# Kernel optimization log

Measured on AMD Instinct MI355X. Metric: run time of the kernel, lower is better.

## Reference

```python
import math
import jax, jax.numpy as jnp
import numpy as np

N = 50000
C = 128      # in_channels == out_channels
H = 8        # nhead
D = C // H   # head_dim = 16
E = 800000


def _layernorm(x, g, b, eps=1e-5):
    mu = jnp.mean(x, axis=-1, keepdims=True)
    var = jnp.var(x, axis=-1, keepdims=True)
    return (x - mu) * jax.lax.rsqrt(var + eps) * g + b


def setup_inputs() -> dict:
    key = jax.random.key(0)
    ks = jax.random.split(key, 12)
    s = 1.0 / math.sqrt(C)          # ~xavier scale
    s4 = 1.0 / math.sqrt(4 * C)
    return {
        "x": jax.random.normal(ks[0], (N, C), dtype=jnp.float32),
        "edge_index": jax.random.randint(ks[1], (2, E), 0, N, dtype=jnp.int64),
        "Wq": jax.random.normal(ks[2], (C, C), dtype=jnp.float32) * s,
        "Wk": jax.random.normal(ks[3], (C, C), dtype=jnp.float32) * s,
        "Wv": jax.random.normal(ks[4], (C, C), dtype=jnp.float32) * s,
        "Wo": jax.random.normal(ks[5], (C, C), dtype=jnp.float32) * s,
        "bo": jnp.zeros((C,), dtype=jnp.float32),
        "Wf1": jax.random.normal(ks[6], (C, 4 * C), dtype=jnp.float32) * s,
        "bf1": jnp.zeros((4 * C,), dtype=jnp.float32),
        "Wf2": jax.random.normal(ks[7], (4 * C, C), dtype=jnp.float32) * s4,
        "bf2": jnp.zeros((C,), dtype=jnp.float32),
        "g1": jnp.ones((C,), dtype=jnp.float32),
        "b1": jnp.zeros((C,), dtype=jnp.float32),
        "g2": jnp.ones((C,), dtype=jnp.float32),
        "b2": jnp.zeros((C,), dtype=jnp.float32),
    }


def reference(x, edge_index, Wq, Wk, Wv, Wo, bo, Wf1, bf1, Wf2, bf2, g1, b1, g2, b2):
    n = x.shape[0]
    loops = jnp.arange(n, dtype=edge_index.dtype)
    row = jnp.concatenate([edge_index[0], loops])  # source nodes
    col = jnp.concatenate([edge_index[1], loops])  # destination nodes

    q = (x @ Wq).reshape(n, H, D)
    k = (x @ Wk).reshape(n, H, D)
    v = (x @ Wv).reshape(n, H, D)

    # edge-level attention scores [E+N, H]
    scores = jnp.einsum('ehd,ehd->eh', q[row], k[col]) / math.sqrt(D)
    smax = jax.ops.segment_max(scores, col, num_segments=n)  # every node has a self-loop
    exp = jnp.exp(scores - smax[col])
    ssum = jax.ops.segment_sum(exp, col, num_segments=n)
    alpha = exp / (ssum[col] + 1e-8)

    out = jax.ops.segment_sum(v[row] * alpha[..., None], col, num_segments=n)
    attn = out.reshape(n, C) @ Wo + bo

    residual = x  # input_proj is Identity (in_channels == out_channels)
    x1 = _layernorm(residual + attn, g1, b1)
    ffn = jax.nn.gelu(x1 @ Wf1 + bf1, approximate=False) @ Wf2 + bf2
    return _layernorm(x1 + ffn, g2, b2)
```

## Files before the change

kernel.cpp:

```cpp
#include <hip/hip_runtime.h>
#include <cmath>


typedef short bf16x8 __attribute__((ext_vector_type(8)));
typedef float f32x4 __attribute__((ext_vector_type(4)));
typedef unsigned int uint_as1 __attribute__((address_space(1)));
typedef unsigned int uint_as3 __attribute__((address_space(3)));

__device__ inline unsigned short f2bf(float f) {
    unsigned int u = __float_as_uint(f);
    u += 0x7fffu + ((u >> 16) & 1u);
    return (unsigned short)(u >> 16);
}
__device__ inline float bflo(unsigned int w) { return __uint_as_float(w << 16); }
__device__ inline float bfhi(unsigned int w) { return __uint_as_float(w & 0xffff0000u); }

__device__ inline void gload16(const unsigned short* g, unsigned short* l) {
    __builtin_amdgcn_global_load_lds((const uint_as1*)g, (uint_as3*)l, 16, 0, 0);
}


__global__ void k_zero(int* __restrict__ p, int n) {
    int i = blockIdx.x * 256 + threadIdx.x;
    if (i < n) p[i] = 0;
}

__global__ void k_count(const int* __restrict__ ei, int* __restrict__ counts,
                        int E, int N) {
    int e = blockIdx.x * 256 + threadIdx.x;
    if (e >= E + N) return;
    int col = (e < E) ? ei[E + e] : (e - E);
    atomicAdd(&counts[col], 1);
}

__global__ void k_scan1(const int* __restrict__ counts, int* __restrict__ incl,
                        int* __restrict__ bsums, int N) {
    __shared__ int s[256];
    int t = threadIdx.x, i = blockIdx.x * 256 + t;
    int v = (i < N) ? counts[i] : 0;
    s[t] = v; __syncthreads();
    for (int off = 1; off < 256; off <<= 1) {
        int add = (t >= off) ? s[t - off] : 0;
        __syncthreads();
        s[t] += add;
        __syncthreads();
    }
    if (i < N) incl[i] = s[t];
    if (t == 255) bsums[blockIdx.x] = s[255];
}

__global__ void k_scan2(const int* __restrict__ bsums, int* __restrict__ boffs, int NB) {
    __shared__ int s[256];
    int t = threadIdx.x;
    int v = (t < NB) ? bsums[t] : 0;
    s[t] = v; __syncthreads();
    for (int off = 1; off < 256; off <<= 1) {
        int add = (t >= off) ? s[t - off] : 0;
        __syncthreads();
        s[t] += add;
        __syncthreads();
    }
    if (t < NB) boffs[t] = s[t] - v;
}

__global__ void k_scan3(const int* __restrict__ incl, const int* __restrict__ counts,
                        const int* __restrict__ boffs, int* __restrict__ nstart,
                        int* __restrict__ cursor, int N) {
    int i = blockIdx.x * 256 + threadIdx.x;
    if (i >= N) return;
    int st = incl[i] - counts[i] + boffs[blockIdx.x];
    nstart[i] = st;
    cursor[i] = st;
}

__global__ void k_fill(const int* __restrict__ ei, int* __restrict__ cursor,
                       int* __restrict__ csr, int E, int N) {
    int e = blockIdx.x * 256 + threadIdx.x;
    if (e >= E + N) return;
    int row, col;
    if (e < E) { row = ei[e]; col = ei[E + e]; }
    else       { row = col = e - E; }
    int pos = atomicAdd(&cursor[col], 1);
    csr[pos] = row;
}


__global__ void k_cast(const float* __restrict__ x, unsigned short* __restrict__ xb,
                       int total4) {
    int i = blockIdx.x * 256 + threadIdx.x;
    if (i >= total4) return;
    float4 v = ((const float4*)x)[i];
    ushort4 o;
    o.x = f2bf(v.x); o.y = f2bf(v.y); o.z = f2bf(v.z); o.w = f2bf(v.w);
    ((ushort4*)xb)[i] = o;
}

__global__ void k_prep(const float* Wq, const float* Wk, const float* Wv, const float* Wo,
                       const float* Wf1, const float* Wf2,
                       unsigned short* Wqkvt, unsigned short* Wot,
                       unsigned short* Wf1t, unsigned short* Wf2t) {
    int z = blockIdx.y;
    const float* in; unsigned short* out; int K, Co;
    switch (z) {
        case 0: in = Wq;  out = Wqkvt;          K = 128; Co = 128; break;
        case 1: in = Wk;  out = Wqkvt + 16384;  K = 128; Co = 128; break;
        case 2: in = Wv;  out = Wqkvt + 32768;  K = 128; Co = 128; break;
        case 3: in = Wo;  out = Wot;            K = 128; Co = 128; break;
        case 4: in = Wf1; out = Wf1t;           K = 128; Co = 512; break;
        default: in = Wf2; out = Wf2t;          K = 512; Co = 128; break;
    }
    int idx = blockIdx.x * 256 + threadIdx.x;
    if (idx >= K * Co) return;
    int k = idx / Co, c = idx % Co;
    out[c * K + k] = f2bf(in[idx]);
}


template <int EPI>
__global__ __launch_bounds__(256) void k_gemm_big(
    const unsigned short* __restrict__ A, const unsigned short* __restrict__ Bt,
    const float* __restrict__ bias, const float* __restrict__ resid,
    const float* __restrict__ g, const float* __restrict__ b,
    float* __restrict__ outf, unsigned short* __restrict__ outb,
    int M, int K, int Cout) {
    __shared__ unsigned short As[128 * 64];
    __shared__ unsigned short Bs[128 * 64];
    __shared__ float pSum[2][128];
    __shared__ float pSq[2][128];

    int tid = threadIdx.x;
    int wid = tid >> 6, lane = tid & 63;
    int quad = lane >> 4, l16 = lane & 15;
    int wr = wid >> 1, wc = wid & 1;
    int m0 = blockIdx.x * 128;
    int n0 = blockIdx.y * 128;

    int srow = tid >> 3;
    int gch = (tid & 7) ^ (srow & 7);
    const unsigned short* gA[4];
    const unsigned short* gB[4];
#pragma unroll
    for (int j = 0; j < 4; ++j) {
        int ra = m0 + j * 32 + srow; if (ra > M - 1) ra = M - 1;
        gA[j] = A + (size_t)ra * K + gch * 8;
        gB[j] = Bt + (size_t)(n0 + j * 32 + srow) * K + gch * 8;
    }

    f32x4 acc[4][4];
#pragma unroll
    for (int i = 0; i < 4; ++i)
#pragma unroll
        for (int j = 0; j < 4; ++j) acc[i][j] = {0.f, 0.f, 0.f, 0.f};

    int KT = K >> 6;
    for (int kt = 0; kt < KT; ++kt) {
        int ko = kt * 64;
#pragma unroll
        for (int j = 0; j < 4; ++j) {
            gload16(gA[j] + ko, As + j * 2048 + tid * 8);
            gload16(gB[j] + ko, Bs + j * 2048 + tid * 8);
        }
        __syncthreads();
#pragma unroll
        for (int s = 0; s < 2; ++s) {
            int swz = ((s * 4 + quad) ^ (l16 & 7)) * 8;
            bf16x8 af[4], bfr[4];
#pragma unroll
            for (int t4 = 0; t4 < 4; ++t4) {
                af[t4]  = *(const bf16x8*)&As[(wr * 64 + t4 * 16 + l16) * 64 + swz];
                bfr[t4] = *(const bf16x8*)&Bs[(wc * 64 + t4 * 16 + l16) * 64 + swz];
            }
#pragma unroll
            for (int ti = 0; ti < 4; ++ti)
#pragma unroll
                for (int tj = 0; tj < 4; ++tj)
                    acc[ti][tj] = __builtin_amdgcn_mfma_f32_16x16x32_bf16(
                        af[ti], bfr[tj], acc[ti][tj], 0, 0, 0);
        }
        __syncthreads();
    }

    if constexpr (EPI != 2) {
#pragma unroll
        for (int ti = 0; ti < 4; ++ti)
#pragma unroll
            for (int tj = 0; tj < 4; ++tj) {
                int col = n0 + wc * 64 + tj * 16 + l16;
#pragma unroll
                for (int r = 0; r < 4; ++r) {
                    int row = m0 + wr * 64 + ti * 16 + quad * 4 + r;
                    if (row >= M) continue;
                    float v = acc[ti][tj][r];
                    if constexpr (EPI == 1) {
                        float gg = v + bias[col];
                        v = 0.5f * gg * (1.f + erff(gg * 0.70710678118f));
                    }
                    outb[(size_t)row * Cout + col] = f2bf(v);
                }
            }
    } else {
        float bi[4], gv[4], bv[4];
#pragma unroll
        for (int tj = 0; tj < 4; ++tj) {
            int col = wc * 64 + tj * 16 + l16;
            bi[tj] = bias[col]; gv[tj] = g[col]; bv[tj] = b[col];
        }
#pragma unroll
        for (int ti = 0; ti < 4; ++ti)
#pragma unroll
            for (int tj = 0; tj < 4; ++tj) {
                int col = wc * 64 + tj * 16 + l16;
#pragma unroll
                for (int r = 0; r < 4; ++r) {
                    int row = m0 + wr * 64 + ti * 16 + quad * 4 + r;
                    float rv = (row < M) ? resid[(size_t)row * 128 + col] : 0.f;
                    acc[ti][tj][r] += bi[tj] + rv;
                }
            }
#pragma unroll
        for (int ti = 0; ti < 4; ++ti)
#pragma unroll
            for (int r = 0; r < 4; ++r) {
                float s = acc[ti][0][r] + acc[ti][1][r] + acc[ti][2][r] + acc[ti][3][r];
                float q = acc[ti][0][r] * acc[ti][0][r] + acc[ti][1][r] * acc[ti][1][r]
                        + acc[ti][2][r] * acc[ti][2][r] + acc[ti][3][r] * acc[ti][3][r];
                s += __shfl_xor(s, 1); q += __shfl_xor(q, 1);
                s += __shfl_xor(s, 2); q += __shfl_xor(q, 2);
                s += __shfl_xor(s, 4); q += __shfl_xor(q, 4);
                s += __shfl_xor(s, 8); q += __shfl_xor(q, 8);
                if (l16 == 0) {
                    int lr = wr * 64 + ti * 16 + quad * 4 + r;
                    pSum[wc][lr] = s; pSq[wc][lr] = q;
                }
            }
        __syncthreads();
        if (tid < 128) {
            float s = pSum[0][tid] + pSum[1][tid];
            float q = pSq[0][tid] + pSq[1][tid];
            float mean = s * 0.0078125f;
            float var = q * 0.0078125f - mean * mean;
            pSum[0][tid] = mean;
            pSq[0][tid] = rsqrtf(var + 1e-5f);
        }
        __syncthreads();
#pragma unroll
        for (int ti = 0; ti < 4; ++ti)
#pragma unroll
            for (int r = 0; r < 4; ++r) {
                int lr = wr * 64 + ti * 16 + quad * 4 + r;
                int row = m0 + lr;
                if (row >= M) continue;
                float mean = pSum[0][lr], rs = pSq[0][lr];
#pragma unroll
                for (int tj = 0; tj < 4; ++tj) {
                    int col = wc * 64 + tj * 16 + l16;
                    float y = (acc[ti][tj][r] - mean) * rs * gv[tj] + bv[tj];
                    if (outf) outf[(size_t)row * 128 + col] = y;
                    if (outb) outb[(size_t)row * 128 + col] = f2bf(y);
                }
            }
    }
}


__global__ __launch_bounds__(256) void k_attn(
    const unsigned int* __restrict__ qkv, const int* __restrict__ nstart,
    const int* __restrict__ counts, const int* __restrict__ csr,
    unsigned int* __restrict__ ob, int N) {
    int j = blockIdx.x * 4 + (threadIdx.x >> 6);
    if (j >= N) return;
    int l = threadIdx.x & 63;

    unsigned int kw = qkv[(size_t)j * 192 + 64 + l];
    float kx = bflo(kw), ky = bfhi(kw);

    int start = nstart[j], cnt = counts[j];
    float m = -3.0e38f, lsum = 0.f, a0 = 0.f, a1 = 0.f;
    int i = 0;
    for (; i + 4 <= cnt; i += 4) {
        int r0 = csr[start + i + 0], r1 = csr[start + i + 1];
        int r2 = csr[start + i + 2], r3 = csr[start + i + 3];
        unsigned int qw0 = qkv[(size_t)r0 * 192 + l];
        unsigned int qw1 = qkv[(size_t)r1 * 192 + l];
        unsigned int qw2 = qkv[(size_t)r2 * 192 + l];
        unsigned int qw3 = qkv[(size_t)r3 * 192 + l];
        unsigned int vw0 = qkv[(size_t)r0 * 192 + 128 + l];
        unsigned int vw1 = qkv[(size_t)r1 * 192 + 128 + l];
        unsigned int vw2 = qkv[(size_t)r2 * 192 + 128 + l];
        unsigned int vw3 = qkv[(size_t)r3 * 192 + 128 + l];

        float p0 = fmaf(bflo(qw0), kx, bfhi(qw0) * ky);
        float p1 = fmaf(bflo(qw1), kx, bfhi(qw1) * ky);
        float p2 = fmaf(bflo(qw2), kx, bfhi(qw2) * ky);
        float p3 = fmaf(bflo(qw3), kx, bfhi(qw3) * ky);
        p0 += __shfl_xor(p0, 1); p1 += __shfl_xor(p1, 1);
        p2 += __shfl_xor(p2, 1); p3 += __shfl_xor(p3, 1);
        p0 += __shfl_xor(p0, 2); p1 += __shfl_xor(p1, 2);
        p2 += __shfl_xor(p2, 2); p3 += __shfl_xor(p3, 2);
        p0 += __shfl_xor(p0, 4); p1 += __shfl_xor(p1, 4);
        p2 += __shfl_xor(p2, 4); p3 += __shfl_xor(p3, 4);
        float s0 = p0 * 0.25f, s1 = p1 * 0.25f, s2 = p2 * 0.25f, s3 = p3 * 0.25f;

        float mn = fmaxf(fmaxf(fmaxf(s0, s1), fmaxf(s2, s3)), m);
        float scale = __expf(m - mn);
        float e0 = __expf(s0 - mn), e1 = __expf(s1 - mn);
        float e2 = __expf(s2 - mn), e3 = __expf(s3 - mn);
        lsum = lsum * scale + ((e0 + e1) + (e2 + e3));
        a0 = a0 * scale + e0 * bflo(vw0) + e1 * bflo(vw1) + e2 * bflo(vw2) + e3 * bflo(vw3);
        a1 = a1 * scale + e0 * bfhi(vw0) + e1 * bfhi(vw1) + e2 * bfhi(vw2) + e3 * bfhi(vw3);
        m = mn;
    }
    for (; i < cnt; ++i) {
        int r = csr[start + i];
        unsigned int qw = qkv[(size_t)r * 192 + l];
        unsigned int vw = qkv[(size_t)r * 192 + 128 + l];
        float p = fmaf(bflo(qw), kx, bfhi(qw) * ky);
        p += __shfl_xor(p, 1);
        p += __shfl_xor(p, 2);
        p += __shfl_xor(p, 4);
        float sc = p * 0.25f;
        float mn = fmaxf(m, sc);
        float scale = __expf(m - mn);
        float e = __expf(sc - mn);
        lsum = lsum * scale + e;
        a0 = a0 * scale + e * bflo(vw);
        a1 = a1 * scale + e * bfhi(vw);
        m = mn;
    }
    float inv = 1.f / (lsum + 1e-8f);
    unsigned int w = ((unsigned int)f2bf(a1 * inv) << 16) | (unsigned int)f2bf(a0 * inv);
    ob[(size_t)j * 64 + l] = w;
}


extern "C" void kernel_launch(void* const* d_in, const int* in_sizes, int n_in,
                              void* d_out, int out_size, void* d_ws, size_t ws_size,
                              hipStream_t stream) {
    const float* x   = (const float*)d_in[0];
    const int* ei    = (const int*)d_in[1];
    const float* Wq  = (const float*)d_in[2];
    const float* Wk  = (const float*)d_in[3];
    const float* Wv  = (const float*)d_in[4];
    const float* Wo  = (const float*)d_in[5];
    const float* bo  = (const float*)d_in[6];
    const float* Wf1 = (const float*)d_in[7];
    const float* bf1 = (const float*)d_in[8];
    const float* Wf2 = (const float*)d_in[9];
    const float* bf2 = (const float*)d_in[10];
    const float* g1  = (const float*)d_in[11];
    const float* b1  = (const float*)d_in[12];
    const float* g2  = (const float*)d_in[13];
    const float* b2  = (const float*)d_in[14];

    int N = in_sizes[0] / 128;
    int E = in_sizes[1] / 2;
    int N2 = ((N + 127) / 128) * 128;
    int NE = E + N;

    char* p = (char*)d_ws;
    auto alloc = [&](size_t bytes) -> char* {
        char* r = p;
        p += (bytes + 255) & ~(size_t)255;
        return r;
    };
    unsigned short* qkv = (unsigned short*)alloc((size_t)N2 * 512 * 2);
    unsigned short* ob  = qkv + (size_t)N2 * 384;
    unsigned short* hb  = qkv;
    unsigned short* x1b = (unsigned short*)alloc((size_t)N2 * 128 * 2);
    unsigned short* xb  = x1b;
    float* x1f          = (float*)alloc((size_t)N2 * 128 * 4);
    unsigned short* Wqkvt = (unsigned short*)alloc(3 * 128 * 128 * 2);
    unsigned short* Wot   = (unsigned short*)alloc(128 * 128 * 2);
    unsigned short* Wf1t  = (unsigned short*)alloc(512 * 128 * 2);
    unsigned short* Wf2t  = (unsigned short*)alloc(128 * 512 * 2);
    int* counts = (int*)alloc((size_t)N * 4);
    int* incl   = (int*)alloc((size_t)N * 4);
    int* nstart = (int*)alloc((size_t)N * 4);
    int* cursor = (int*)alloc((size_t)N * 4);
    int* bsums  = (int*)alloc(1024 * 4);
    int* boffs  = (int*)alloc(1024 * 4);
    int* csr    = (int*)alloc((size_t)NE * 4);

    int NB = (N + 255) / 256;
    int M128 = (N + 127) / 128;

    k_zero<<<NB, 256, 0, stream>>>(counts, N);
    k_count<<<(NE + 255) / 256, 256, 0, stream>>>(ei, counts, E, N);
    k_scan1<<<NB, 256, 0, stream>>>(counts, incl, bsums, N);
    k_scan2<<<1, 256, 0, stream>>>(bsums, boffs, NB);
    k_scan3<<<NB, 256, 0, stream>>>(incl, counts, boffs, nstart, cursor, N);
    k_fill<<<(NE + 255) / 256, 256, 0, stream>>>(ei, cursor, csr, E, N);

    k_cast<<<((N * 128 / 4) + 255) / 256, 256, 0, stream>>>(x, xb, N * 128 / 4);
    k_prep<<<dim3(256, 6), 256, 0, stream>>>(Wq, Wk, Wv, Wo, Wf1, Wf2,
                                             Wqkvt, Wot, Wf1t, Wf2t);

    k_gemm_big<0><<<dim3(M128, 3), 256, 0, stream>>>(
        xb, Wqkvt, nullptr, nullptr, nullptr, nullptr, nullptr, qkv, N, 128, 384);

    k_attn<<<(N + 3) / 4, 256, 0, stream>>>((const unsigned int*)qkv, nstart,
                                            counts, csr, (unsigned int*)ob, N);

    k_gemm_big<2><<<dim3(M128, 1), 256, 0, stream>>>(
        ob, Wot, bo, x, g1, b1, x1f, x1b, N, 128, 128);

    k_gemm_big<1><<<dim3(M128, 4), 256, 0, stream>>>(
        x1b, Wf1t, bf1, nullptr, nullptr, nullptr, nullptr, hb, N, 128, 512);

    k_gemm_big<2><<<dim3(M128, 1), 256, 0, stream>>>(
        hb, Wf2t, bf2, x1f, g2, b2, (float*)d_out, nullptr, N, 512, 128);
}
```

Measured before the change: 387.0 us.

## Fuse FFN up/down GEMMs into one kernel keeping hidden activations in LDS

```diff
diff --git a/kernel.cpp b/kernel.cpp
--- a/kernel.cpp
+++ b/kernel.cpp
@@ -17,6 +17,12 @@
 
 __device__ inline void gload16(const unsigned short* g, unsigned short* l) {
     __builtin_amdgcn_global_load_lds((const uint_as1*)g, (uint_as3*)l, 16, 0, 0);
+}
+
+__device__ inline bf16x8 ldfrag(const unsigned short* t, int row, int ks, int quad) {
+    int ch = (ks & 1) * 4 + quad;
+    int pos = ch ^ (row & 7);
+    return *(const bf16x8*)&t[((ks >> 1) << 13) + row * 64 + pos * 8];
 }
 
 
@@ -117,14 +123,13 @@
 
 
 template <int EPI>
-__global__ __launch_bounds__(256) void k_gemm_big(
+__global__ __launch_bounds__(256) void k_gemm128(
     const unsigned short* __restrict__ A, const unsigned short* __restrict__ Bt,
     const float* __restrict__ bias, const float* __restrict__ resid,
     const float* __restrict__ g, const float* __restrict__ b,
     float* __restrict__ outf, unsigned short* __restrict__ outb,
-    int M, int K, int Cout) {
-    __shared__ unsigned short As[128 * 64];
-    __shared__ unsigned short Bs[128 * 64];
+    int M, int Cout) {
+    __shared__ unsigned short As[16384];
     __shared__ float pSum[2][128];
     __shared__ float pSq[2][128];
 
@@ -135,16 +140,23 @@
     int m0 = blockIdx.x * 128;
     int n0 = blockIdx.y * 128;
 
-    int srow = tid >> 3;
-    int gch = (tid & 7) ^ (srow & 7);
-    const unsigned short* gA[4];
-    const unsigned short* gB[4];
-#pragma unroll
-    for (int j = 0; j < 4; ++j) {
-        int ra = m0 + j * 32 + srow; if (ra > M - 1) ra = M - 1;
-        gA[j] = A + (size_t)ra * K + gch * 8;
-        gB[j] = Bt + (size_t)(n0 + j * 32 + srow) * K + gch * 8;
-    }
+    int rsub = lane >> 3, ch = lane & 7;
+    int gch = ch ^ rsub;
+#pragma unroll
+    for (int kt = 0; kt < 2; ++kt)
+#pragma unroll
+        for (int j = 0; j < 4; ++j) {
+            int row = j * 32 + wid * 8 + rsub;
+            int ra = m0 + row; if (ra > M - 1) ra = M - 1;
+            gload16(A + (size_t)ra * 128 + kt * 64 + gch * 8,
+                    As + kt * 8192 + j * 2048 + wid * 512 + lane * 8);
+        }
+    __syncthreads();
+
+    const bf16x8* Brow[4];
+#pragma unroll
+    for (int tj = 0; tj < 4; ++tj)
+        Brow[tj] = (const bf16x8*)(Bt + (size_t)(n0 + wc * 64 + tj * 16 + l16) * 128);
 
     f32x4 acc[4][4];
 #pragma unroll
@@ -152,32 +164,21 @@
 #pragma unroll
         for (int j = 0; j < 4; ++j) acc[i][j] = {0.f, 0.f, 0.f, 0.f};
 
-    int KT = K >> 6;
-    for (int kt = 0; kt < KT; ++kt) {
-        int ko = kt * 64;
-#pragma unroll
-        for (int j = 0; j < 4; ++j) {
-            gload16(gA[j] + ko, As + j * 2048 + tid * 8);
-            gload16(gB[j] + ko, Bs + j * 2048 + tid * 8);
-        }
-        __syncthreads();
-#pragma unroll
-        for (int s = 0; s < 2; ++s) {
-            int swz = ((s * 4 + quad) ^ (l16 & 7)) * 8;
-            bf16x8 af[4], bfr[4];
-#pragma unroll
-            for (int t4 = 0; t4 < 4; ++t4) {
-                af[t4]  = *(const bf16x8*)&As[(wr * 64 + t4 * 16 + l16) * 64 + swz];
-                bfr[t4] = *(const bf16x8*)&Bs[(wc * 64 + t4 * 16 + l16) * 64 + swz];
-            }
-#pragma unroll
-            for (int ti = 0; ti < 4; ++ti)
-#pragma unroll
-                for (int tj = 0; tj < 4; ++tj)
-                    acc[ti][tj] = __builtin_amdgcn_mfma_f32_16x16x32_bf16(
-                        af[ti], bfr[tj], acc[ti][tj], 0, 0, 0);
-        }
-        __syncthreads();
+#pragma unroll
+    for (int ks = 0; ks < 4; ++ks) {
+        bf16x8 af[4], bfr[4];
+#pragma unroll
+        for (int t4 = 0; t4 < 4; ++t4)
+            af[t4] = ldfrag(As, wr * 64 + t4 * 16 + l16, ks, quad);
+#pragma unroll
+        for (int tj = 0; tj < 4; ++tj)
+            bfr[tj] = Brow[tj][ks * 4 + quad];
+#pragma unroll
+        for (int ti = 0; ti < 4; ++ti)
+#pragma unroll
+            for (int tj = 0; tj < 4; ++tj)
+                acc[ti][tj] = __builtin_amdgcn_mfma_f32_16x16x32_bf16(
+                    af[ti], bfr[tj], acc[ti][tj], 0, 0, 0);
     }
 
     if constexpr (EPI != 2) {
@@ -190,12 +191,7 @@
                 for (int r = 0; r < 4; ++r) {
                     int row = m0 + wr * 64 + ti * 16 + quad * 4 + r;
                     if (row >= M) continue;
-                    float v = acc[ti][tj][r];
-                    if constexpr (EPI == 1) {
-                        float gg = v + bias[col];
-                        v = 0.5f * gg * (1.f + erff(gg * 0.70710678118f));
-                    }
-                    outb[(size_t)row * Cout + col] = f2bf(v);
+                    outb[(size_t)row * Cout + col] = f2bf(acc[ti][tj][r]);
                 }
             }
     } else {
@@ -260,6 +256,164 @@
                 }
             }
     }
+}
+
+
+__global__ __launch_bounds__(512) void k_ffn(
+    const unsigned short* __restrict__ x1b, const unsigned short* __restrict__ Wf1t,
+    const float* __restrict__ bf1, const unsigned short* __restrict__ Wf2t,
+    const float* __restrict__ bf2, const float* __restrict__ x1f,
+    const float* __restrict__ g2, const float* __restrict__ b2,
+    float* __restrict__ outp, int M) {
+    __shared__ unsigned short As[16384];
+    __shared__ unsigned short Hs[16384];
+
+    int tid = threadIdx.x;
+    int wid = tid >> 6, lane = tid & 63;
+    int quad = lane >> 4, l16 = lane & 15;
+    int wr = wid >> 2;
+    int wc = wid & 3;
+    int m0 = blockIdx.x * 128;
+
+    int rsub = lane >> 3, ch = lane & 7;
+    int gch = ch ^ rsub;
+#pragma unroll
+    for (int kt = 0; kt < 2; ++kt)
+#pragma unroll
+        for (int j = 0; j < 2; ++j) {
+            int row = j * 64 + wid * 8 + rsub;
+            int ra = m0 + row; if (ra > M - 1) ra = M - 1;
+            gload16(x1b + (size_t)ra * 128 + kt * 64 + gch * 8,
+                    As + kt * 8192 + j * 4096 + wid * 512 + lane * 8);
+        }
+
+    f32x4 oacc[4][2];
+#pragma unroll
+    for (int i = 0; i < 4; ++i) { oacc[i][0] = {0.f,0.f,0.f,0.f}; oacc[i][1] = oacc[i][0]; }
+
+    for (int c = 0; c < 4; ++c) {
+        __syncthreads();
+        f32x4 hacc[4][2];
+#pragma unroll
+        for (int i = 0; i < 4; ++i) { hacc[i][0] = {0.f,0.f,0.f,0.f}; hacc[i][1] = hacc[i][0]; }
+        const bf16x8* B1row[2];
+#pragma unroll
+        for (int u = 0; u < 2; ++u)
+            B1row[u] = (const bf16x8*)(Wf1t + (size_t)(c * 128 + wc * 32 + u * 16 + l16) * 128);
+#pragma unroll
+        for (int ks = 0; ks < 4; ++ks) {
+            bf16x8 af[4], bfr[2];
+#pragma unroll
+            for (int t4 = 0; t4 < 4; ++t4)
+                af[t4] = ldfrag(As, wr * 64 + t4 * 16 + l16, ks, quad);
+#pragma unroll
+            for (int u = 0; u < 2; ++u) bfr[u] = B1row[u][ks * 4 + quad];
+#pragma unroll
+            for (int t4 = 0; t4 < 4; ++t4)
+#pragma unroll
+                for (int u = 0; u < 2; ++u)
+                    hacc[t4][u] = __builtin_amdgcn_mfma_f32_16x16x32_bf16(
+                        af[t4], bfr[u], hacc[t4][u], 0, 0, 0);
+        }
+        float b1v[2];
+#pragma unroll
+        for (int u = 0; u < 2; ++u) b1v[u] = bf1[c * 128 + wc * 32 + u * 16 + l16];
+#pragma unroll
+        for (int t4 = 0; t4 < 4; ++t4)
+#pragma unroll
+            for (int u = 0; u < 2; ++u) {
+                int k = wc * 32 + u * 16 + l16;
+                int kt = k >> 6, kk = k & 63;
+#pragma unroll
+                for (int r = 0; r < 4; ++r) {
+                    int row = wr * 64 + t4 * 16 + quad * 4 + r;
+                    float gg = hacc[t4][u][r] + b1v[u];
+                    float y = 0.5f * gg * (1.f + erff(gg * 0.70710678118f));
+                    int pos = (kk >> 3) ^ (row & 7);
+                    Hs[kt * 8192 + row * 64 + pos * 8 + (kk & 7)] = f2bf(y);
+                }
+            }
+        __syncthreads();
+        const bf16x8* B2row[2];
+#pragma unroll
+        for (int u = 0; u < 2; ++u)
+            B2row[u] = (const bf16x8*)(Wf2t + (size_t)(wc * 32 + u * 16 + l16) * 512 + c * 128);
+#pragma unroll
+        for (int ks = 0; ks < 4; ++ks) {
+            bf16x8 af[4], bfr[2];
+#pragma unroll
+            for (int t4 = 0; t4 < 4; ++t4)
+                af[t4] = ldfrag(Hs, wr * 64 + t4 * 16 + l16, ks, quad);
+#pragma unroll
+            for (int u = 0; u < 2; ++u) bfr[u] = B2row[u][ks * 4 + quad];
+#pragma unroll
+            for (int t4 = 0; t4 < 4; ++t4)
+#pragma unroll
+                for (int u = 0; u < 2; ++u)
+                    oacc[t4][u] = __builtin_amdgcn_mfma_f32_16x16x32_bf16(
+                        af[t4], bfr[u], oacc[t4][u], 0, 0, 0);
+        }
+    }
+    __syncthreads();
+    float* pS = (float*)Hs;
+    float* pQ = pS + 512;
+    float* mv = pQ + 512;
+
+    float b2v[2], gv[2], bv[2];
+#pragma unroll
+    for (int u = 0; u < 2; ++u) {
+        int col = wc * 32 + u * 16 + l16;
+        b2v[u] = bf2[col]; gv[u] = g2[col]; bv[u] = b2[col];
+    }
+#pragma unroll
+    for (int t4 = 0; t4 < 4; ++t4)
+#pragma unroll
+        for (int u = 0; u < 2; ++u) {
+            int col = wc * 32 + u * 16 + l16;
+#pragma unroll
+            for (int r = 0; r < 4; ++r) {
+                int row = m0 + wr * 64 + t4 * 16 + quad * 4 + r;
+                float rv = (row < M) ? x1f[(size_t)row * 128 + col] : 0.f;
+                oacc[t4][u][r] += b2v[u] + rv;
+            }
+        }
+#pragma unroll
+    for (int t4 = 0; t4 < 4; ++t4)
+#pragma unroll
+        for (int r = 0; r < 4; ++r) {
+            int lr = wr * 64 + t4 * 16 + quad * 4 + r;
+            float s = oacc[t4][0][r] + oacc[t4][1][r];
+            float q = oacc[t4][0][r] * oacc[t4][0][r] + oacc[t4][1][r] * oacc[t4][1][r];
+            s += __shfl_xor(s, 1); q += __shfl_xor(q, 1);
+            s += __shfl_xor(s, 2); q += __shfl_xor(q, 2);
+            s += __shfl_xor(s, 4); q += __shfl_xor(q, 4);
+            s += __shfl_xor(s, 8); q += __shfl_xor(q, 8);
+            if (l16 == 0) { pS[wc * 128 + lr] = s; pQ[wc * 128 + lr] = q; }
+        }
+    __syncthreads();
+    if (tid < 128) {
+        float s = pS[tid] + pS[128 + tid] + pS[256 + tid] + pS[384 + tid];
+        float q = pQ[tid] + pQ[128 + tid] + pQ[256 + tid] + pQ[384 + tid];
+        float mean = s * 0.0078125f;
+        float var = q * 0.0078125f - mean * mean;
+        mv[tid] = mean;
+        mv[128 + tid] = rsqrtf(var + 1e-5f);
+    }
+    __syncthreads();
+#pragma unroll
+    for (int t4 = 0; t4 < 4; ++t4)
+#pragma unroll
+        for (int r = 0; r < 4; ++r) {
+            int lr = wr * 64 + t4 * 16 + quad * 4 + r;
+            int row = m0 + lr;
+            if (row >= M) continue;
+            float mean = mv[lr], rs = mv[128 + lr];
+#pragma unroll
+            for (int u = 0; u < 2; ++u) {
+                int col = wc * 32 + u * 16 + l16;
+                outp[(size_t)row * 128 + col] = (oacc[t4][u][r] - mean) * rs * gv[u] + bv[u];
+            }
+        }
 }
 
 
@@ -365,7 +519,6 @@
     };
     unsigned short* qkv = (unsigned short*)alloc((size_t)N2 * 512 * 2);
     unsigned short* ob  = qkv + (size_t)N2 * 384;
-    unsigned short* hb  = qkv;
     unsigned short* x1b = (unsigned short*)alloc((size_t)N2 * 128 * 2);
     unsigned short* xb  = x1b;
     float* x1f          = (float*)alloc((size_t)N2 * 128 * 4);
@@ -395,18 +548,15 @@
     k_prep<<<dim3(256, 6), 256, 0, stream>>>(Wq, Wk, Wv, Wo, Wf1, Wf2,
                                              Wqkvt, Wot, Wf1t, Wf2t);
 
-    k_gemm_big<0><<<dim3(M128, 3), 256, 0, stream>>>(
-        xb, Wqkvt, nullptr, nullptr, nullptr, nullptr, nullptr, qkv, N, 128, 384);
+    k_gemm128<0><<<dim3(M128, 3), 256, 0, stream>>>(
+        xb, Wqkvt, nullptr, nullptr, nullptr, nullptr, nullptr, qkv, N, 384);
 
     k_attn<<<(N + 3) / 4, 256, 0, stream>>>((const unsigned int*)qkv, nstart,
                                             counts, csr, (unsigned int*)ob, N);
 
-    k_gemm_big<2><<<dim3(M128, 1), 256, 0, stream>>>(
-        ob, Wot, bo, x, g1, b1, x1f, x1b, N, 128, 128);
-
-    k_gemm_big<1><<<dim3(M128, 4), 256, 0, stream>>>(
-        x1b, Wf1t, bf1, nullptr, nullptr, nullptr, nullptr, hb, N, 128, 512);
-
-    k_gemm_big<2><<<dim3(M128, 1), 256, 0, stream>>>(
-        hb, Wf2t, bf2, x1f, g2, b2, (float*)d_out, nullptr, N, 512, 128);
-}
+    k_gemm128<2><<<dim3(M128, 1), 256, 0, stream>>>(
+        ob, Wot, bo, x, g1, b1, x1f, x1b, N, 128);
+
+    k_ffn<<<dim3(M128), 512, 0, stream>>>(
+        x1b, Wf1t, bf1, Wf2t, bf2, x1f, g2, b2, (float*)d_out, N);
+}
```

Result: no change. 391.0 us (+1.0%).

## Replace LDS-tiled 128x128 GEMMs with register-resident-weight 32-row streaming kernels

Applied to the files above, without the earlier changes.

```diff
diff --git a/kernel.cpp b/kernel.cpp
--- a/kernel.cpp
+++ b/kernel.cpp
@@ -4,8 +4,6 @@
 
 typedef short bf16x8 __attribute__((ext_vector_type(8)));
 typedef float f32x4 __attribute__((ext_vector_type(4)));
-typedef unsigned int uint_as1 __attribute__((address_space(1)));
-typedef unsigned int uint_as3 __attribute__((address_space(3)));
 
 __device__ inline unsigned short f2bf(float f) {
     unsigned int u = __float_as_uint(f);
@@ -14,10 +12,6 @@
 }
 __device__ inline float bflo(unsigned int w) { return __uint_as_float(w << 16); }
 __device__ inline float bfhi(unsigned int w) { return __uint_as_float(w & 0xffff0000u); }
-
-__device__ inline void gload16(const unsigned short* g, unsigned short* l) {
-    __builtin_amdgcn_global_load_lds((const uint_as1*)g, (uint_as3*)l, 16, 0, 0);
-}
 
 
 __global__ void k_zero(int* __restrict__ p, int n) {
@@ -116,150 +110,240 @@
 }
 
 
-template <int EPI>
-__global__ __launch_bounds__(256) void k_gemm_big(
+__device__ inline void load_breg(const unsigned short* __restrict__ Bt, int n0,
+                                 int l16, int quad, bf16x8 Breg[4][4]) {
+#pragma unroll
+    for (int tj = 0; tj < 4; ++tj) {
+        const bf16x8* Br = (const bf16x8*)(Bt + (size_t)(n0 + tj * 16 + l16) * 128);
+#pragma unroll
+        for (int ks = 0; ks < 4; ++ks) Breg[ks][tj] = Br[ks * 4 + quad];
+    }
+}
+
+__device__ inline void mfma_strip(const unsigned short* __restrict__ A, int m0, int M,
+                                  int l16, int quad, const bf16x8 Breg[4][4],
+                                  f32x4 acc[2][4]) {
+    int ra0 = m0 + l16;      if (ra0 > M - 1) ra0 = M - 1;
+    int ra1 = m0 + 16 + l16; if (ra1 > M - 1) ra1 = M - 1;
+    const bf16x8* A0 = (const bf16x8*)(A + (size_t)ra0 * 128);
+    const bf16x8* A1 = (const bf16x8*)(A + (size_t)ra1 * 128);
+#pragma unroll
+    for (int ks = 0; ks < 4; ++ks) {
+        bf16x8 a0 = A0[ks * 4 + quad];
+        bf16x8 a1 = A1[ks * 4 + quad];
+#pragma unroll
+        for (int tj = 0; tj < 4; ++tj) {
+            acc[0][tj] = __builtin_amdgcn_mfma_f32_16x16x32_bf16(a0, Breg[ks][tj], acc[0][tj], 0, 0, 0);
+            acc[1][tj] = __builtin_amdgcn_mfma_f32_16x16x32_bf16(a1, Breg[ks][tj], acc[1][tj], 0, 0, 0);
+        }
+    }
+}
+
+
+template <int EPI, int NW>
+__global__ __launch_bounds__(NW * 64) void k_stream(
+    const unsigned short* __restrict__ A, const unsigned short* __restrict__ Bt,
+    const float* __restrict__ bias, unsigned short* __restrict__ outb,
+    int M, int Cout) {
+    int tid = threadIdx.x;
+    int wid = tid >> 6, lane = tid & 63;
+    int quad = lane >> 4, l16 = lane & 15;
+    int m0 = blockIdx.x * 32;
+    int n0 = blockIdx.y * (NW * 64) + wid * 64;
+
+    bf16x8 Breg[4][4];
+    load_breg(Bt, n0, l16, quad, Breg);
+
+    f32x4 acc[2][4];
+#pragma unroll
+    for (int i = 0; i < 2; ++i)
+#pragma unroll
+        for (int j = 0; j < 4; ++j) acc[i][j] = {0.f, 0.f, 0.f, 0.f};
+
+    mfma_strip(A, m0, M, l16, quad, Breg, acc);
+
+#pragma unroll
+    for (int ti = 0; ti < 2; ++ti)
+#pragma unroll
+        for (int tj = 0; tj < 4; ++tj) {
+            int col = n0 + tj * 16 + l16;
+            float bi = (EPI == 1) ? bias[col] : 0.f;
+#pragma unroll
+            for (int r = 0; r < 4; ++r) {
+                int row = m0 + ti * 16 + quad * 4 + r;
+                if (row >= M) continue;
+                float v = acc[ti][tj][r];
+                if constexpr (EPI == 1) {
+                    float gg = v + bi;
+                    v = 0.5f * gg * (1.f + erff(gg * 0.70710678118f));
+                }
+                outb[(size_t)row * Cout + col] = f2bf(v);
+            }
+        }
+}
+
+
+__global__ __launch_bounds__(128) void k_woln(
     const unsigned short* __restrict__ A, const unsigned short* __restrict__ Bt,
     const float* __restrict__ bias, const float* __restrict__ resid,
     const float* __restrict__ g, const float* __restrict__ b,
-    float* __restrict__ outf, unsigned short* __restrict__ outb,
-    int M, int K, int Cout) {
-    __shared__ unsigned short As[128 * 64];
-    __shared__ unsigned short Bs[128 * 64];
-    __shared__ float pSum[2][128];
-    __shared__ float pSq[2][128];
-
+    float* __restrict__ outf, unsigned short* __restrict__ outb, int M) {
+    __shared__ float pS[2][32], pQ[2][32];
     int tid = threadIdx.x;
     int wid = tid >> 6, lane = tid & 63;
     int quad = lane >> 4, l16 = lane & 15;
-    int wr = wid >> 1, wc = wid & 1;
-    int m0 = blockIdx.x * 128;
-    int n0 = blockIdx.y * 128;
-
-    int srow = tid >> 3;
-    int gch = (tid & 7) ^ (srow & 7);
-    const unsigned short* gA[4];
-    const unsigned short* gB[4];
-#pragma unroll
-    for (int j = 0; j < 4; ++j) {
-        int ra = m0 + j * 32 + srow; if (ra > M - 1) ra = M - 1;
-        gA[j] = A + (size_t)ra * K + gch * 8;
-        gB[j] = Bt + (size_t)(n0 + j * 32 + srow) * K + gch * 8;
-    }
-
-    f32x4 acc[4][4];
-#pragma unroll
-    for (int i = 0; i < 4; ++i)
+    int m0 = blockIdx.x * 32;
+    int n0 = wid * 64;
+
+    bf16x8 Breg[4][4];
+    load_breg(Bt, n0, l16, quad, Breg);
+    f32x4 acc[2][4];
+#pragma unroll
+    for (int i = 0; i < 2; ++i)
 #pragma unroll
         for (int j = 0; j < 4; ++j) acc[i][j] = {0.f, 0.f, 0.f, 0.f};
-
-    int KT = K >> 6;
-    for (int kt = 0; kt < KT; ++kt) {
-        int ko = kt * 64;
-#pragma unroll
-        for (int j = 0; j < 4; ++j) {
-            gload16(gA[j] + ko, As + j * 2048 + tid * 8);
-            gload16(gB[j] + ko, Bs + j * 2048 + tid * 8);
-        }
-        __syncthreads();
-#pragma unroll
-        for (int s = 0; s < 2; ++s) {
-            int swz = ((s * 4 + quad) ^ (l16 & 7)) * 8;
-            bf16x8 af[4], bfr[4];
-#pragma unroll
-            for (int t4 = 0; t4 < 4; ++t4) {
-                af[t4]  = *(const bf16x8*)&As[(wr * 64 + t4 * 16 + l16) * 64 + swz];
-                bfr[t4] = *(const bf16x8*)&Bs[(wc * 64 + t4 * 16 + l16) * 64 + swz];
-            }
-#pragma unroll
-            for (int ti = 0; ti < 4; ++ti)
-#pragma unroll
-                for (int tj = 0; tj < 4; ++tj)
-                    acc[ti][tj] = __builtin_amdgcn_mfma_f32_16x16x32_bf16(
-                        af[ti], bfr[tj], acc[ti][tj], 0, 0, 0);
-        }
-        __syncthreads();
-    }
-
-    if constexpr (EPI != 2) {
-#pragma unroll
-        for (int ti = 0; ti < 4; ++ti)
-#pragma unroll
-            for (int tj = 0; tj < 4; ++tj) {
-                int col = n0 + wc * 64 + tj * 16 + l16;
-#pragma unroll
-                for (int r = 0; r < 4; ++r) {
-                    int row = m0 + wr * 64 + ti * 16 + quad * 4 + r;
-                    if (row >= M) continue;
-                    float v = acc[ti][tj][r];
-                    if constexpr (EPI == 1) {
-                        float gg = v + bias[col];
-                        v = 0.5f * gg * (1.f + erff(gg * 0.70710678118f));
-                    }
-                    outb[(size_t)row * Cout + col] = f2bf(v);
-                }
-            }
-    } else {
-        float bi[4], gv[4], bv[4];
-#pragma unroll
-        for (int tj = 0; tj < 4; ++tj) {
-            int col = wc * 64 + tj * 16 + l16;
-            bi[tj] = bias[col]; gv[tj] = g[col]; bv[tj] = b[col];
-        }
-#pragma unroll
-        for (int ti = 0; ti < 4; ++ti)
-#pragma unroll
-            for (int tj = 0; tj < 4; ++tj) {
-                int col = wc * 64 + tj * 16 + l16;
-#pragma unroll
-                for (int r = 0; r < 4; ++r) {
-                    int row = m0 + wr * 64 + ti * 16 + quad * 4 + r;
-                    float rv = (row < M) ? resid[(size_t)row * 128 + col] : 0.f;
-                    acc[ti][tj][r] += bi[tj] + rv;
-                }
-            }
-#pragma unroll
-        for (int ti = 0; ti < 4; ++ti)
+    mfma_strip(A, m0, M, l16, quad, Breg, acc);
+
+#pragma unroll
+    for (int tj = 0; tj < 4; ++tj) {
+        int col = n0 + tj * 16 + l16;
+        float bi = bias[col];
+#pragma unroll
+        for (int ti = 0; ti < 2; ++ti)
 #pragma unroll
             for (int r = 0; r < 4; ++r) {
-                float s = acc[ti][0][r] + acc[ti][1][r] + acc[ti][2][r] + acc[ti][3][r];
-                float q = acc[ti][0][r] * acc[ti][0][r] + acc[ti][1][r] * acc[ti][1][r]
-                        + acc[ti][2][r] * acc[ti][2][r] + acc[ti][3][r] * acc[ti][3][r];
-                s += __shfl_xor(s, 1); q += __shfl_xor(q, 1);
-                s += __shfl_xor(s, 2); q += __shfl_xor(q, 2);
-                s += __shfl_xor(s, 4); q += __shfl_xor(q, 4);
-                s += __shfl_xor(s, 8); q += __shfl_xor(q, 8);
-                if (l16 == 0) {
-                    int lr = wr * 64 + ti * 16 + quad * 4 + r;
-                    pSum[wc][lr] = s; pSq[wc][lr] = q;
-                }
-            }
-        __syncthreads();
-        if (tid < 128) {
-            float s = pSum[0][tid] + pSum[1][tid];
-            float q = pSq[0][tid] + pSq[1][tid];
+                int row = m0 + ti * 16 + quad * 4 + r;
+                float rv = (row < M) ? resid[(size_t)row * 128 + col] : 0.f;
+                acc[ti][tj][r] += bi + rv;
+            }
+    }
+#pragma unroll
+    for (int ti = 0; ti < 2; ++ti)
+#pragma unroll
+        for (int r = 0; r < 4; ++r) {
+            float s = acc[ti][0][r] + acc[ti][1][r] + acc[ti][2][r] + acc[ti][3][r];
+            float q = acc[ti][0][r] * acc[ti][0][r] + acc[ti][1][r] * acc[ti][1][r]
+                    + acc[ti][2][r] * acc[ti][2][r] + acc[ti][3][r] * acc[ti][3][r];
+            s += __shfl_xor(s, 1); q += __shfl_xor(q, 1);
+            s += __shfl_xor(s, 2); q += __shfl_xor(q, 2);
+            s += __shfl_xor(s, 4); q += __shfl_xor(q, 4);
+            s += __shfl_xor(s, 8); q += __shfl_xor(q, 8);
+            if (l16 == 0) {
+                int lr = ti * 16 + quad * 4 + r;
+                pS[wid][lr] = s; pQ[wid][lr] = q;
+            }
+        }
+    __syncthreads();
+#pragma unroll
+    for (int ti = 0; ti < 2; ++ti)
+#pragma unroll
+        for (int r = 0; r < 4; ++r) {
+            int lr = ti * 16 + quad * 4 + r;
+            int row = m0 + lr;
+            if (row >= M) continue;
+            float s = pS[0][lr] + pS[1][lr];
+            float q = pQ[0][lr] + pQ[1][lr];
             float mean = s * 0.0078125f;
             float var = q * 0.0078125f - mean * mean;
-            pSum[0][tid] = mean;
-            pSq[0][tid] = rsqrtf(var + 1e-5f);
-        }
-        __syncthreads();
-#pragma unroll
-        for (int ti = 0; ti < 4; ++ti)
+            float rs = rsqrtf(var + 1e-5f);
+#pragma unroll
+            for (int tj = 0; tj < 4; ++tj) {
+                int col = n0 + tj * 16 + l16;
+                float y = (acc[ti][tj][r] - mean) * rs * g[col] + b[col];
+                outf[(size_t)row * 128 + col] = y;
+                outb[(size_t)row * 128 + col] = f2bf(y);
+            }
+        }
+}
+
+
+__global__ __launch_bounds__(128) void k_ffn2ln(
+    const unsigned short* __restrict__ A, const unsigned short* __restrict__ Bt,
+    const float* __restrict__ bias, const float* __restrict__ resid,
+    const float* __restrict__ g, const float* __restrict__ b,
+    float* __restrict__ outp, int M) {
+    __shared__ float pS[2][32], pQ[2][32];
+    int tid = threadIdx.x;
+    int wid = tid >> 6, lane = tid & 63;
+    int quad = lane >> 4, l16 = lane & 15;
+    int m0 = blockIdx.x * 32;
+    int n0 = wid * 64;
+
+    int ra0 = m0 + l16;      if (ra0 > M - 1) ra0 = M - 1;
+    int ra1 = m0 + 16 + l16; if (ra1 > M - 1) ra1 = M - 1;
+    const bf16x8* A0 = (const bf16x8*)(A + (size_t)ra0 * 512);
+    const bf16x8* A1 = (const bf16x8*)(A + (size_t)ra1 * 512);
+    const bf16x8* Brow[4];
+#pragma unroll
+    for (int tj = 0; tj < 4; ++tj)
+        Brow[tj] = (const bf16x8*)(Bt + (size_t)(n0 + tj * 16 + l16) * 512);
+
+    f32x4 acc[2][4];
+#pragma unroll
+    for (int i = 0; i < 2; ++i)
+#pragma unroll
+        for (int j = 0; j < 4; ++j) acc[i][j] = {0.f, 0.f, 0.f, 0.f};
+
+#pragma unroll 4
+    for (int ks = 0; ks < 16; ++ks) {
+        bf16x8 a0 = A0[ks * 4 + quad];
+        bf16x8 a1 = A1[ks * 4 + quad];
+#pragma unroll
+        for (int tj = 0; tj < 4; ++tj) {
+            bf16x8 bf = Brow[tj][ks * 4 + quad];
+            acc[0][tj] = __builtin_amdgcn_mfma_f32_16x16x32_bf16(a0, bf, acc[0][tj], 0, 0, 0);
+            acc[1][tj] = __builtin_amdgcn_mfma_f32_16x16x32_bf16(a1, bf, acc[1][tj], 0, 0, 0);
+        }
+    }
+
+#pragma unroll
+    for (int tj = 0; tj < 4; ++tj) {
+        int col = n0 + tj * 16 + l16;
+        float bi = bias[col];
+#pragma unroll
+        for (int ti = 0; ti < 2; ++ti)
 #pragma unroll
             for (int r = 0; r < 4; ++r) {
-                int lr = wr * 64 + ti * 16 + quad * 4 + r;
-                int row = m0 + lr;
-                if (row >= M) continue;
-                float mean = pSum[0][lr], rs = pSq[0][lr];
-#pragma unroll
-                for (int tj = 0; tj < 4; ++tj) {
-                    int col = wc * 64 + tj * 16 + l16;
-                    float y = (acc[ti][tj][r] - mean) * rs * gv[tj] + bv[tj];
-                    if (outf) outf[(size_t)row * 128 + col] = y;
-                    if (outb) outb[(size_t)row * 128 + col] = f2bf(y);
-                }
-            }
-    }
+                int row = m0 + ti * 16 + quad * 4 + r;
+                float rv = (row < M) ? resid[(size_t)row * 128 + col] : 0.f;
+                acc[ti][tj][r] += bi + rv;
+            }
+    }
+#pragma unroll
+    for (int ti = 0; ti < 2; ++ti)
+#pragma unroll
+        for (int r = 0; r < 4; ++r) {
+            float s = acc[ti][0][r] + acc[ti][1][r] + acc[ti][2][r] + acc[ti][3][r];
+            float q = acc[ti][0][r] * acc[ti][0][r] + acc[ti][1][r] * acc[ti][1][r]
+                    + acc[ti][2][r] * acc[ti][2][r] + acc[ti][3][r] * acc[ti][3][r];
+            s += __shfl_xor(s, 1); q += __shfl_xor(q, 1);
+            s += __shfl_xor(s, 2); q += __shfl_xor(q, 2);
+            s += __shfl_xor(s, 4); q += __shfl_xor(q, 4);
+            s += __shfl_xor(s, 8); q += __shfl_xor(q, 8);
+            if (l16 == 0) {
+                int lr = ti * 16 + quad * 4 + r;
+                pS[wid][lr] = s; pQ[wid][lr] = q;
+            }
+        }
+    __syncthreads();
+#pragma unroll
+    for (int ti = 0; ti < 2; ++ti)
+#pragma unroll
+        for (int r = 0; r < 4; ++r) {
+            int lr = ti * 16 + quad * 4 + r;
+            int row = m0 + lr;
+            if (row >= M) continue;
+            float s = pS[0][lr] + pS[1][lr];
+            float q = pQ[0][lr] + pQ[1][lr];
+            float mean = s * 0.0078125f;
+            float var = q * 0.0078125f - mean * mean;
+            float rs = rsqrtf(var + 1e-5f);
+#pragma unroll
+            for (int tj = 0; tj < 4; ++tj) {
+                int col = n0 + tj * 16 + l16;
+                outp[(size_t)row * 128 + col] = (acc[ti][tj][r] - mean) * rs * g[col] + b[col];
+            }
+        }
 }
 
 
@@ -354,7 +438,7 @@
 
     int N = in_sizes[0] / 128;
     int E = in_sizes[1] / 2;
-    int N2 = ((N + 127) / 128) * 128;
+    int N2 = ((N + 31) / 32) * 32;
     int NE = E + N;
 
     char* p = (char*)d_ws;
@@ -382,7 +466,7 @@
     int* csr    = (int*)alloc((size_t)NE * 4);
 
     int NB = (N + 255) / 256;
-    int M128 = (N + 127) / 128;
+    int M32 = (N + 31) / 32;
 
     k_zero<<<NB, 256, 0, stream>>>(counts, N);
     k_count<<<(NE + 255) / 256, 256, 0, stream>>>(ei, counts, E, N);
@@ -395,18 +479,15 @@
     k_prep<<<dim3(256, 6), 256, 0, stream>>>(Wq, Wk, Wv, Wo, Wf1, Wf2,
                                              Wqkvt, Wot, Wf1t, Wf2t);
 
-    k_gemm_big<0><<<dim3(M128, 3), 256, 0, stream>>>(
-        xb, Wqkvt, nullptr, nullptr, nullptr, nullptr, nullptr, qkv, N, 128, 384);
+    k_stream<0, 3><<<dim3(M32, 2), 192, 0, stream>>>(xb, Wqkvt, nullptr, qkv, N, 384);
 
     k_attn<<<(N + 3) / 4, 256, 0, stream>>>((const unsigned int*)qkv, nstart,
                                             counts, csr, (unsigned int*)ob, N);
 
-    k_gemm_big<2><<<dim3(M128, 1), 256, 0, stream>>>(
-        ob, Wot, bo, x, g1, b1, x1f, x1b, N, 128, 128);
-
-    k_gemm_big<1><<<dim3(M128, 4), 256, 0, stream>>>(
-        x1b, Wf1t, bf1, nullptr, nullptr, nullptr, nullptr, hb, N, 128, 512);
-
-    k_gemm_big<2><<<dim3(M128, 1), 256, 0, stream>>>(
-        hb, Wf2t, bf2, x1f, g2, b2, (float*)d_out, nullptr, N, 512, 128);
-}
+    k_woln<<<dim3(M32), 128, 0, stream>>>(ob, Wot, bo, x, g1, b1, x1f, x1b, N);
+
+    k_stream<1, 4><<<dim3(M32, 2), 256, 0, stream>>>(x1b, Wf1t, bf1, hb, N, 512);
+
+    k_ffn2ln<<<dim3(M32), 128, 0, stream>>>(hb, Wf2t, bf2, x1f, g2, b2,
+                                            (float*)d_out, N);
+}
```

After: 422.1 us. 9.1% more time.
